# Kernel tuning notes

Measured on AMD Instinct MI355X. Metric: run time of the kernel, lower is better.

## Reference

```python
import jax, jax.numpy as jnp
import numpy as np

B, S, D, H = 2, 2048, 1024, 16
HD = D // H
DFF = 4096
EPS = 1e-5


def layernorm(x, w, b):
    m = jnp.mean(x, axis=-1, keepdims=True)
    v = jnp.mean((x - m) ** 2, axis=-1, keepdims=True)
    return (x - m) / jnp.sqrt(v + EPS) * w + b


def setup_inputs() -> dict:
    key = jax.random.key(0)
    ks = jax.random.split(key, 5)
    s = 0.02  # init scale for weights
    return {
        "src": jax.random.normal(ks[0], (B, S, D), jnp.float32),
        "norm_w": jnp.ones((D,), jnp.float32),
        "norm_b": jnp.zeros((D,), jnp.float32),
        "wqkv_w": jax.random.normal(ks[1], (D, 3 * D), jnp.float32) * s,
        "wqkv_b": jnp.zeros((3 * D,), jnp.float32),
        "out_w": jax.random.normal(ks[2], (D, D), jnp.float32) * s,
        "out_b": jnp.zeros((D,), jnp.float32),
        "fnorm_w": jnp.ones((D,), jnp.float32),
        "fnorm_b": jnp.zeros((D,), jnp.float32),
        "ff1_w": jax.random.normal(ks[3], (D, DFF), jnp.float32) * s,
        "ff1_b": jnp.zeros((DFF,), jnp.float32),
        "ff2_w": jax.random.normal(ks[4], (DFF, D), jnp.float32) * s,
        "ff2_b": jnp.zeros((D,), jnp.float32),
    }


def reference(src, norm_w, norm_b, wqkv_w, wqkv_b, out_w, out_b,
              fnorm_w, fnorm_b, ff1_w, ff1_b, ff2_w, ff2_b):
    bs, seq, dim = src.shape
    hd = dim // H
    qkv = layernorm(src, norm_w, norm_b) @ wqkv_w + wqkv_b  # [b,s,3d]
    qkv = qkv.reshape(bs, seq, 3, H, hd).transpose(2, 0, 3, 1, 4)  # [3,b,h,s,hd]
    q, k, v = qkv[0], qkv[1], qkv[2]
    # ALiBi bias: (j - i) * 2^{-h}, -inf above diagonal (causal)
    i = jnp.arange(seq)[:, None]
    j = jnp.arange(seq)[None, :]
    slopes = 2.0 ** (-jnp.arange(H, dtype=jnp.float32))  # [h]
    rel = (j - i).astype(jnp.float32)  # [s,s]
    bias = slopes[:, None, None] * rel[None]  # [h,s,s]
    bias = jnp.where((j > i)[None], -jnp.inf, bias)
    scale = 1.0 / jnp.sqrt(jnp.asarray(hd, jnp.float32))
    scores = jnp.einsum("bhqd,bhkd->bhqk", q, k) * scale + bias[None]
    attn = jax.nn.softmax(scores, axis=-1)
    ctx = jnp.einsum("bhqk,bhkd->bhqd", attn, v)
    ctx = ctx.transpose(0, 2, 1, 3).reshape(bs, seq, dim)
    src = src + ctx @ out_w + out_b
    h = layernorm(src, fnorm_w, fnorm_b)
    ff = jax.nn.relu(h @ ff1_w + ff1_b) @ ff2_w + ff2_b
    return src + ff
```

## Files before the change

### kernel.cpp

```cpp
#include <hip/hip_runtime.h>
#include <math.h>

#define S_   2048
#define D_   1024
#define H_   16
#define DFF_ 4096

#define NEGINF (-__builtin_huge_valf())

typedef __bf16 bf16x8 __attribute__((ext_vector_type(8)));
typedef float  f32x4  __attribute__((ext_vector_type(4)));

static __device__ __forceinline__ unsigned short f2bf_rne(float f) {
    unsigned int u = __float_as_uint(f);
    u = (u + 0x7fffu + ((u >> 16) & 1u)) >> 16;
    return (unsigned short)u;
}

template<bool OBF>
__global__ __launch_bounds__(256) void ln_kernel(
    const float* __restrict__ x, const float* __restrict__ w,
    const float* __restrict__ b, void* __restrict__ y)
{
    const int row = blockIdx.x;
    const int t = threadIdx.x;
    const float4 v = reinterpret_cast<const float4*>(x + (size_t)row * D_)[t];
    float s  = v.x + v.y + v.z + v.w;
    float ss = v.x*v.x + v.y*v.y + v.z*v.z + v.w*v.w;
    #pragma unroll
    for (int o = 32; o; o >>= 1) {
        s  += __shfl_xor(s,  o, 64);
        ss += __shfl_xor(ss, o, 64);
    }
    __shared__ float red[8];
    const int wid = t >> 6, lane = t & 63;
    if (lane == 0) { red[wid] = s; red[4 + wid] = ss; }
    __syncthreads();
    s  = red[0] + red[1] + red[2] + red[3];
    ss = red[4] + red[5] + red[6] + red[7];
    const float mean = s * (1.f / D_);
    const float var  = ss * (1.f / D_) - mean * mean;
    const float rstd = rsqrtf(var + 1e-5f);
    const float4 wv = reinterpret_cast<const float4*>(w)[t];
    const float4 bv = reinterpret_cast<const float4*>(b)[t];
    float4 o;
    o.x = (v.x - mean) * rstd * wv.x + bv.x;
    o.y = (v.y - mean) * rstd * wv.y + bv.y;
    o.z = (v.z - mean) * rstd * wv.z + bv.z;
    o.w = (v.w - mean) * rstd * wv.w + bv.w;
    if (OBF) {
        ushort4 o4;
        o4.x = f2bf_rne(o.x); o4.y = f2bf_rne(o.y);
        o4.z = f2bf_rne(o.z); o4.w = f2bf_rne(o.w);
        reinterpret_cast<ushort4*>((unsigned short*)y + (size_t)row * D_)[t] = o4;
    } else {
        reinterpret_cast<float4*>((float*)y + (size_t)row * D_)[t] = o;
    }
}

__global__ __launch_bounds__(256) void wcast_kernel(
    const float* __restrict__ in, unsigned short* __restrict__ outT, int K, int N)
{
    __shared__ float t[64][65];
    const int n0 = blockIdx.x * 64, k0 = blockIdx.y * 64;
    const int tid = threadIdx.x;
    #pragma unroll
    for (int i = 0; i < 16; ++i) {
        const int idx = i * 256 + tid;
        const int kk = idx >> 6, nn = idx & 63;
        t[kk][nn] = in[(size_t)(k0 + kk) * N + n0 + nn];
    }
    __syncthreads();
    #pragma unroll
    for (int i = 0; i < 16; ++i) {
        const int idx = i * 256 + tid;
        const int nn = idx >> 6, kk = idx & 63;
        outT[(size_t)(n0 + nn) * K + k0 + kk] = f2bf_rne(t[kk][nn]);
    }
}

template<int EPI, bool OBF>
__global__ __launch_bounds__(256) void bgemm_kernel(
    const __bf16* __restrict__ A,
    const __bf16* __restrict__ Bt,
    const float* __restrict__ bias, const float* __restrict__ res,
    void* __restrict__ Cv, int M, int N, int K)
{
    __shared__ __align__(16) __bf16 As[128 * 32];
    __shared__ __align__(16) __bf16 Bs[128 * 32];
    const int tid  = threadIdx.x;
    const int w    = tid >> 6, lane = tid & 63;
    const int wr   = w >> 1, wc = w & 1;
    const int row0 = blockIdx.y * 128, col0 = blockIdx.x * 128;

    const int lrow = lane >> 2;
    const int lchk = (lane & 3) * 8;
    const int frow = lane & 15;
    const int fk   = (lane >> 4) * 8;

    f32x4 acc[4][4] = {};

    for (int kt = 0; kt < K; kt += 32) {
        #pragma unroll
        for (int it = 0; it < 2; ++it) {
            const int arow = w * 32 + it * 16;
            __builtin_amdgcn_global_load_lds(
                (__attribute__((address_space(1))) void*)(A + (size_t)(row0 + arow + lrow) * K + kt + lchk),
                (__attribute__((address_space(3))) void*)(&As[arow * 32]), 16, 0, 0);
            __builtin_amdgcn_global_load_lds(
                (__attribute__((address_space(1))) void*)(Bt + (size_t)(col0 + arow + lrow) * K + kt + lchk),
                (__attribute__((address_space(3))) void*)(&Bs[arow * 32]), 16, 0, 0);
        }
        __syncthreads();
        bf16x8 af[4], bfr[4];
        #pragma unroll
        for (int i = 0; i < 4; ++i) {
            af[i]  = *(const bf16x8*)&As[(wr * 64 + i * 16 + frow) * 32 + fk];
            bfr[i] = *(const bf16x8*)&Bs[(wc * 64 + i * 16 + frow) * 32 + fk];
        }
        #pragma unroll
        for (int mi = 0; mi < 4; ++mi)
            #pragma unroll
            for (int ni = 0; ni < 4; ++ni)
                acc[mi][ni] = __builtin_amdgcn_mfma_f32_16x16x32_bf16(
                    af[mi], bfr[ni], acc[mi][ni], 0, 0, 0);
        __syncthreads();
    }

    float bz[4];
    #pragma unroll
    for (int ni = 0; ni < 4; ++ni) bz[ni] = bias[col0 + wc * 64 + ni * 16 + frow];
    #pragma unroll
    for (int mi = 0; mi < 4; ++mi) {
        #pragma unroll
        for (int j = 0; j < 4; ++j) {
            const int row = row0 + wr * 64 + mi * 16 + (lane >> 4) * 4 + j;
            #pragma unroll
            for (int ni = 0; ni < 4; ++ni) {
                const int col = col0 + wc * 64 + ni * 16 + frow;
                float v = acc[mi][ni][j] + bz[ni];
                if (EPI == 1) v = fmaxf(v, 0.f);
                if (EPI == 2) v += res[(size_t)row * N + col];
                if (OBF) ((unsigned short*)Cv)[(size_t)row * N + col] = f2bf_rne(v);
                else     ((float*)Cv)[(size_t)row * N + col] = v;
            }
        }
    }
}

__global__ __launch_bounds__(256) void attn_kernel(
    const __bf16* __restrict__ qkv, __bf16* __restrict__ ctx)
{
    const int pair = blockIdx.x & 15;
    const int bh   = blockIdx.x >> 4;
    const int b    = bh >> 4, h = bh & 15;
    const int tid  = threadIdx.x;
    const int wid  = tid >> 6, lane = tid & 63;
    const int l15  = lane & 15, l4 = lane >> 4;
    const float slope = exp2f(-(float)h);
    const size_t rowb = (size_t)b * S_;

    __shared__ __align__(16) __bf16 Ks[64 * 72];
    __shared__ __align__(16) __bf16 Vt[64 * 72];
    __shared__ __align__(16) __bf16 Ps[4 * 16 * 72];

    const int jr = tid >> 3;
    const int c  = tid & 7;
    const int c8 = c * 8;
    __bf16* psw = &Ps[wid * 16 * 72];
    const __bf16* base = qkv + rowb * 3072 + h * 64;

    #pragma unroll 1
    for (int half = 0; half < 2; ++half) {
        const int qt = half ? 31 - pair : pair;
        const int i0 = qt << 6;

        bf16x8 qf[2];
        {
            const __bf16* qp = base + (size_t)(i0 + wid * 16 + l15) * 3072 + l4 * 8;
            qf[0] = *(const bf16x8*)(qp);
            qf[1] = *(const bf16x8*)(qp + 32);
        }

        float m[4], l[4];
        f32x4 acc[4];
        #pragma unroll
        for (int j = 0; j < 4; ++j) { m[j] = NEGINF; l[j] = 0.f; }
        #pragma unroll
        for (int ni = 0; ni < 4; ++ni) acc[ni] = (f32x4){0.f, 0.f, 0.f, 0.f};

        bf16x8 k0, k1, v0, v1;
        {
            const __bf16* kvp = base + (size_t)jr * 3072;
            k0 = *(const bf16x8*)(kvp + 1024 + c8);
            v0 = *(const bf16x8*)(kvp + 2048 + c8);
            k1 = *(const bf16x8*)(kvp + 32 * 3072 + 1024 + c8);
            v1 = *(const bf16x8*)(kvp + 32 * 3072 + 2048 + c8);
        }

        for (int kt = 0; kt <= qt; ++kt) {
            __syncthreads();
            *(bf16x8*)&Ks[jr * 72 + c8]        = k0;
            *(bf16x8*)&Ks[(jr + 32) * 72 + c8] = k1;
            const int sw0 = (((jr >> 3) ^ c) & 7) * 8 + (jr & 7);
            const int sw1 = ((((jr + 32) >> 3) ^ c) & 7) * 8 + (jr & 7);
            #pragma unroll
            for (int e = 0; e < 8; ++e) {
                Vt[(c8 + e) * 72 + sw0] = v0[e];
                Vt[(c8 + e) * 72 + sw1] = v1[e];
            }
            __syncthreads();

            if (kt < qt) {
                const __bf16* kvp = base + (size_t)(((kt + 1) << 6) + jr) * 3072;
                k0 = *(const bf16x8*)(kvp + 1024 + c8);
                v0 = *(const bf16x8*)(kvp + 2048 + c8);
                k1 = *(const bf16x8*)(kvp + 32 * 3072 + 1024 + c8);
                v1 = *(const bf16x8*)(kvp + 32 * 3072 + 2048 + c8);
            }

            f32x4 sf[4];
            #pragma unroll
            for (int ni = 0; ni < 4; ++ni) sf[ni] = (f32x4){0.f, 0.f, 0.f, 0.f};
            #pragma unroll
            for (int kd = 0; kd < 2; ++kd)
                #pragma unroll
                for (int ni = 0; ni < 4; ++ni) {
                    const bf16x8 bf = *(const bf16x8*)&Ks[(ni * 16 + l15) * 72 + kd * 32 + l4 * 8];
                    sf[ni] = __builtin_amdgcn_mfma_f32_16x16x32_bf16(qf[kd], bf, sf[ni], 0, 0, 0);
                }

            float pv[4][4];
            const int j0 = kt << 6;
            if (kt == qt) {
                #pragma unroll
                for (int ni = 0; ni < 4; ++ni) {
                    const int jcol = ni * 16 + l15;
                    #pragma unroll
                    for (int j = 0; j < 4; ++j) {
                        const int iloc = wid * 16 + l4 * 4 + j;
                        pv[ni][j] = (jcol <= iloc)
                            ? fmaf(slope, (float)(jcol - iloc), sf[ni][j] * 0.125f)
                            : NEGINF;
                    }
                }
            } else {
                const float dbase = (float)(j0 - i0);
                #pragma unroll
                for (int ni = 0; ni < 4; ++ni) {
                    const int jcol = ni * 16 + l15;
                    #pragma unroll
                    for (int j = 0; j < 4; ++j) {
                        const int iloc = wid * 16 + l4 * 4 + j;
                        pv[ni][j] = fmaf(slope, dbase + (float)(jcol - iloc), sf[ni][j] * 0.125f);
                    }
                }
            }

            #pragma unroll
            for (int j = 0; j < 4; ++j) {
                float mx = fmaxf(fmaxf(pv[0][j], pv[1][j]), fmaxf(pv[2][j], pv[3][j]));
                mx = fmaxf(mx, __shfl_xor(mx, 1, 64));
                mx = fmaxf(mx, __shfl_xor(mx, 2, 64));
                mx = fmaxf(mx, __shfl_xor(mx, 4, 64));
                mx = fmaxf(mx, __shfl_xor(mx, 8, 64));
                const float mnew = fmaxf(m[j], mx);
                const float corr = __expf(m[j] - mnew);
                float s0 = 0.f;
                #pragma unroll
                for (int ni = 0; ni < 4; ++ni) {
                    const float e = __expf(pv[ni][j] - mnew);
                    pv[ni][j] = e;
                    s0 += e;
                }
                s0 += __shfl_xor(s0, 1, 64);
                s0 += __shfl_xor(s0, 2, 64);
                s0 += __shfl_xor(s0, 4, 64);
                s0 += __shfl_xor(s0, 8, 64);
                l[j] = l[j] * corr + s0;
                m[j] = mnew;
                #pragma unroll
                for (int ni = 0; ni < 4; ++ni) acc[ni][j] *= corr;
            }

            #pragma unroll
            for (int ni = 0; ni < 4; ++ni)
                #pragma unroll
                for (int j = 0; j < 4; ++j)
                    psw[(l4 * 4 + j) * 72 + ni * 16 + l15] = (__bf16)pv[ni][j];
            asm volatile("" ::: "memory");

            #pragma unroll
            for (int kk = 0; kk < 2; ++kk) {
                const bf16x8 pa = *(const bf16x8*)&psw[l15 * 72 + kk * 32 + l4 * 8];
                #pragma unroll
                for (int ni = 0; ni < 4; ++ni) {
                    const int d = ni * 16 + l15;
                    const int pc = ((kk * 4 + l4) ^ (d >> 3)) & 7;
                    const bf16x8 bv = *(const bf16x8*)&Vt[d * 72 + pc * 8];
                    acc[ni] = __builtin_amdgcn_mfma_f32_16x16x32_bf16(pa, bv, acc[ni], 0, 0, 0);
                }
            }
        }

        #pragma unroll
        for (int ni = 0; ni < 4; ++ni) {
            const int col = h * 64 + ni * 16 + l15;
            #pragma unroll
            for (int j = 0; j < 4; ++j) {
                const int row = i0 + wid * 16 + l4 * 4 + j;
                ctx[(rowb + row) * (size_t)D_ + col] = (__bf16)(acc[ni][j] / l[j]);
            }
        }
    }
}

extern "C" void kernel_launch(void* const* d_in, const int* in_sizes, int n_in,
                              void* d_out, int out_size, void* d_ws, size_t ws_size,
                              hipStream_t stream) {
    const float* src     = (const float*)d_in[0];
    const float* norm_w  = (const float*)d_in[1];
    const float* norm_b  = (const float*)d_in[2];
    const float* wqkv_w  = (const float*)d_in[3];
    const float* wqkv_b  = (const float*)d_in[4];
    const float* out_w   = (const float*)d_in[5];
    const float* out_b   = (const float*)d_in[6];
    const float* fnorm_w = (const float*)d_in[7];
    const float* fnorm_b = (const float*)d_in[8];
    const float* ff1_w   = (const float*)d_in[9];
    const float* ff1_b   = (const float*)d_in[10];
    const float* ff2_w   = (const float*)d_in[11];
    const float* ff2_b   = (const float*)d_in[12];
    float* out = (float*)d_out;

    const int M = 2 * S_;
    const size_t MB = 1u << 20;
    char* W = (char*)d_ws;
    unsigned short* wqkvT = (unsigned short*)(W);
    unsigned short* outT  = (unsigned short*)(W + 6  * MB);
    unsigned short* ff1T  = (unsigned short*)(W + 8  * MB);
    unsigned short* ff2T  = (unsigned short*)(W + 16 * MB);
    unsigned short* h1    = (unsigned short*)(W + 24 * MB);
    unsigned short* qkv   = (unsigned short*)(W + 32 * MB);
    unsigned short* ctx   = (unsigned short*)(W + 24 * MB);
    unsigned short* h2    = (unsigned short*)(W + 32 * MB);
    unsigned short* ffmid = (unsigned short*)(W + 40 * MB);
    float*          src2  = (float*)        (W + 80 * MB);

    wcast_kernel<<<dim3(3072/64, 1024/64), 256, 0, stream>>>(wqkv_w, wqkvT, 1024, 3072);
    wcast_kernel<<<dim3(1024/64, 1024/64), 256, 0, stream>>>(out_w,  outT,  1024, 1024);
    wcast_kernel<<<dim3(4096/64, 1024/64), 256, 0, stream>>>(ff1_w,  ff1T,  1024, 4096);
    wcast_kernel<<<dim3(1024/64, 4096/64), 256, 0, stream>>>(ff2_w,  ff2T,  4096, 1024);

    ln_kernel<true><<<M, 256, 0, stream>>>(src, norm_w, norm_b, h1);
    bgemm_kernel<0, true><<<dim3(3072/128, M/128), 256, 0, stream>>>(
        (const __bf16*)h1, (const __bf16*)wqkvT, wqkv_b, nullptr, qkv, M, 3072, 1024);
    attn_kernel<<<2 * H_ * 16, 256, 0, stream>>>((const __bf16*)qkv, (__bf16*)ctx);
    bgemm_kernel<2, false><<<dim3(1024/128, M/128), 256, 0, stream>>>(
        (const __bf16*)ctx, (const __bf16*)outT, out_b, src, src2, M, 1024, 1024);
    ln_kernel<true><<<M, 256, 0, stream>>>(src2, fnorm_w, fnorm_b, h2);
    bgemm_kernel<1, true><<<dim3(4096/128, M/128), 256, 0, stream>>>(
        (const __bf16*)h2, (const __bf16*)ff1T, ff1_b, nullptr, ffmid, M, 4096, 1024);
    bgemm_kernel<2, false><<<dim3(1024/128, M/128), 256, 0, stream>>>(
        (const __bf16*)ffmid, (const __bf16*)ff2T, ff2_b, src2, out, M, 1024, 4096);
}
```

Baseline: 423.7 us.

## Deepen GEMM K-tile to 64, XOR-swizzle LDS, and remap workgroups across XCDs

```diff
diff --git a/kernel.cpp b/kernel.cpp
--- a/kernel.cpp
+++ b/kernel.cpp
@@ -86,44 +86,55 @@
     const float* __restrict__ bias, const float* __restrict__ res,
     void* __restrict__ Cv, int M, int N, int K)
 {
-    __shared__ __align__(16) __bf16 As[128 * 32];
-    __shared__ __align__(16) __bf16 Bs[128 * 32];
+    __shared__ __align__(16) __bf16 As[128 * 64];
+    __shared__ __align__(16) __bf16 Bs[128 * 64];
     const int tid  = threadIdx.x;
     const int w    = tid >> 6, lane = tid & 63;
     const int wr   = w >> 1, wc = w & 1;
-    const int row0 = blockIdx.y * 128, col0 = blockIdx.x * 128;
-
-    const int lrow = lane >> 2;
-    const int lchk = (lane & 3) * 8;
+
+    const int nwg  = gridDim.x;
+    const int lin  = blockIdx.x;
+    const int wg   = (lin & 7) * (nwg >> 3) + (lin >> 3);
+    const int gridN = N >> 7;
+    const int row0 = (wg / gridN) << 7;
+    const int col0 = (wg % gridN) << 7;
+
+    const int srow = lane >> 3;
+    const int scol = ((lane & 7) ^ srow) << 3;
     const int frow = lane & 15;
-    const int fk   = (lane >> 4) * 8;
+    const int l4   = lane >> 4;
+    const int r7   = frow & 7;
 
     f32x4 acc[4][4] = {};
 
-    for (int kt = 0; kt < K; kt += 32) {
-        #pragma unroll
-        for (int it = 0; it < 2; ++it) {
-            const int arow = w * 32 + it * 16;
+    for (int kt = 0; kt < K; kt += 64) {
+        #pragma unroll
+        for (int it = 0; it < 4; ++it) {
+            const int arow = w * 32 + it * 8;
             __builtin_amdgcn_global_load_lds(
-                (__attribute__((address_space(1))) void*)(A + (size_t)(row0 + arow + lrow) * K + kt + lchk),
-                (__attribute__((address_space(3))) void*)(&As[arow * 32]), 16, 0, 0);
+                (__attribute__((address_space(1))) void*)(A + (size_t)(row0 + arow + srow) * K + kt + scol),
+                (__attribute__((address_space(3))) void*)(&As[arow * 64]), 16, 0, 0);
             __builtin_amdgcn_global_load_lds(
-                (__attribute__((address_space(1))) void*)(Bt + (size_t)(col0 + arow + lrow) * K + kt + lchk),
-                (__attribute__((address_space(3))) void*)(&Bs[arow * 32]), 16, 0, 0);
+                (__attribute__((address_space(1))) void*)(Bt + (size_t)(col0 + arow + srow) * K + kt + scol),
+                (__attribute__((address_space(3))) void*)(&Bs[arow * 64]), 16, 0, 0);
         }
         __syncthreads();
-        bf16x8 af[4], bfr[4];
-        #pragma unroll
-        for (int i = 0; i < 4; ++i) {
-            af[i]  = *(const bf16x8*)&As[(wr * 64 + i * 16 + frow) * 32 + fk];
-            bfr[i] = *(const bf16x8*)&Bs[(wc * 64 + i * 16 + frow) * 32 + fk];
-        }
-        #pragma unroll
-        for (int mi = 0; mi < 4; ++mi)
-            #pragma unroll
-            for (int ni = 0; ni < 4; ++ni)
-                acc[mi][ni] = __builtin_amdgcn_mfma_f32_16x16x32_bf16(
-                    af[mi], bfr[ni], acc[mi][ni], 0, 0, 0);
+        #pragma unroll
+        for (int kk = 0; kk < 2; ++kk) {
+            const int ch = ((kk * 4 + l4) ^ r7) * 8;
+            bf16x8 af[4], bfr[4];
+            #pragma unroll
+            for (int i = 0; i < 4; ++i) {
+                af[i]  = *(const bf16x8*)&As[(wr * 64 + i * 16 + frow) * 64 + ch];
+                bfr[i] = *(const bf16x8*)&Bs[(wc * 64 + i * 16 + frow) * 64 + ch];
+            }
+            #pragma unroll
+            for (int mi = 0; mi < 4; ++mi)
+                #pragma unroll
+                for (int ni = 0; ni < 4; ++ni)
+                    acc[mi][ni] = __builtin_amdgcn_mfma_f32_16x16x32_bf16(
+                        af[mi], bfr[ni], acc[mi][ni], 0, 0, 0);
+        }
         __syncthreads();
     }
 
@@ -134,7 +145,7 @@
     for (int mi = 0; mi < 4; ++mi) {
         #pragma unroll
         for (int j = 0; j < 4; ++j) {
-            const int row = row0 + wr * 64 + mi * 16 + (lane >> 4) * 4 + j;
+            const int row = row0 + wr * 64 + mi * 16 + l4 * 4 + j;
             #pragma unroll
             for (int ni = 0; ni < 4; ++ni) {
                 const int col = col0 + wc * 64 + ni * 16 + frow;
@@ -353,14 +364,14 @@
     wcast_kernel<<<dim3(1024/64, 4096/64), 256, 0, stream>>>(ff2_w,  ff2T,  4096, 1024);
 
     ln_kernel<true><<<M, 256, 0, stream>>>(src, norm_w, norm_b, h1);
-    bgemm_kernel<0, true><<<dim3(3072/128, M/128), 256, 0, stream>>>(
+    bgemm_kernel<0, true><<<(3072/128) * (M/128), 256, 0, stream>>>(
         (const __bf16*)h1, (const __bf16*)wqkvT, wqkv_b, nullptr, qkv, M, 3072, 1024);
     attn_kernel<<<2 * H_ * 16, 256, 0, stream>>>((const __bf16*)qkv, (__bf16*)ctx);
-    bgemm_kernel<2, false><<<dim3(1024/128, M/128), 256, 0, stream>>>(
+    bgemm_kernel<2, false><<<(1024/128) * (M/128), 256, 0, stream>>>(
         (const __bf16*)ctx, (const __bf16*)outT, out_b, src, src2, M, 1024, 1024);
     ln_kernel<true><<<M, 256, 0, stream>>>(src2, fnorm_w, fnorm_b, h2);
-    bgemm_kernel<1, true><<<dim3(4096/128, M/128), 256, 0, stream>>>(
+    bgemm_kernel<1, true><<<(4096/128) * (M/128), 256, 0, stream>>>(
         (const __bf16*)h2, (const __bf16*)ff1T, ff1_b, nullptr, ffmid, M, 4096, 1024);
-    bgemm_kernel<2, false><<<dim3(1024/128, M/128), 256, 0, stream>>>(
+    bgemm_kernel<2, false><<<(1024/128) * (M/128), 256, 0, stream>>>(
         (const __bf16*)ffmid, (const __bf16*)ff2T, ff2_b, src2, out, M, 1024, 4096);
 }
```

Result: faster. 411.1 us (-3.0%).
